# Kernel optimization log

Measured on AMD Instinct MI355X. Metric: run time of the kernel, lower is better.

## Reference

```python
import jax, jax.numpy as jnp
import numpy as np

B, T, H = 4, 8192, 512
LN_EPS = 1e-5


def _ln(x, g, b):
    mu = jnp.mean(x, axis=-1, keepdims=True)
    var = jnp.mean((x - mu) ** 2, axis=-1, keepdims=True)
    return (x - mu) * jax.lax.rsqrt(var + LN_EPS) * g + b


def _log_g(x):
    # log of g(x) = x + 0.5 (x >= 0) else sigmoid(x); both branches NaN-safe.
    return jnp.where(x >= 0, jnp.log(jax.nn.relu(x) + 0.5), -jax.nn.softplus(-x))


def _min_gru(x, Wz, bz, Wh, bh):
    # minGRU parallel log-space scan ("Were RNNs All We Needed?" Alg.), h_0 = 0.
    k = x @ Wz + bz                      # [B,T,H] gate pre-activation
    log_z = -jax.nn.softplus(-k)         # log sigmoid(k)
    log_coeffs = -jax.nn.softplus(k)     # log (1 - sigmoid(k))
    log_tilde_h = _log_g(x @ Wh + bh)
    log_h0 = jnp.full((x.shape[0], 1, x.shape[2]), jnp.log(0.5), x.dtype)  # g(0)=0.5
    log_values = jnp.concatenate([log_h0, log_z + log_tilde_h], axis=1)   # [B,T+1,H]
    a_star = jnp.cumsum(jnp.pad(log_coeffs, ((0, 0), (1, 0), (0, 0))), axis=1)
    log_h = a_star + jax.lax.cumlogsumexp(log_values - a_star, axis=1)
    return jnp.exp(log_h)[:, 1:]         # drop h_0 slot -> [B,T,H]


def setup_inputs() -> dict:
    key = jax.random.key(0)
    ks = jax.random.split(key, 5)
    s = 1.0 / np.sqrt(H)
    return {
        "x": jax.random.normal(ks[0], (B, T, H), jnp.float32),
        "ln1_g": jnp.ones((H,), jnp.float32),
        "ln1_b": jnp.zeros((H,), jnp.float32),
        "Wz": jax.random.normal(ks[1], (H, H), jnp.float32) * s,
        "bz": jnp.zeros((H,), jnp.float32),
        "Wh": jax.random.normal(ks[2], (H, H), jnp.float32) * s,
        "bh": jnp.zeros((H,), jnp.float32),
        "ln2_g": jnp.ones((H,), jnp.float32),
        "ln2_b": jnp.zeros((H,), jnp.float32),
        "W1": jax.random.normal(ks[3], (H, H), jnp.float32) * s,
        "b1": jnp.zeros((H,), jnp.float32),
        "W2": jax.random.normal(ks[4], (H, H), jnp.float32) * s,
        "b2": jnp.zeros((H,), jnp.float32),
    }


def reference(x, ln1_g, ln1_b, Wz, bz, Wh, bh, ln2_g, ln2_b, W1, b1, W2, b2):
    # x = x + minGRU(ln_1(x))   (dropout=0 -> identity)
    x = x + _min_gru(_ln(x, ln1_g, ln1_b), Wz, bz, Wh, bh)
    # x = x + FFN(ln_2(x)) ; FFN = Linear -> ReLU -> Linear (hidden->hidden)
    h = jax.nn.relu(_ln(x, ln2_g, ln2_b) @ W1 + b1)
    x = x + (h @ W2 + b2)
    return x
```

## Files before the change

### kernel.cpp

```cpp
#include <hip/hip_runtime.h>

typedef unsigned short u16;
typedef unsigned int u32;
typedef __bf16 bf16x8 __attribute__((ext_vector_type(8)));
typedef float f32x4 __attribute__((ext_vector_type(4)));
typedef u16 u16x8 __attribute__((ext_vector_type(8)));

__device__ __forceinline__ u16 f2bf(float f) {
    union { float f; u32 i; } v; v.f = f;
    u32 x = v.i;
    u32 r = (x + 0x7fffu + ((x >> 16) & 1u)) >> 16;
    return (u16)r;
}
__device__ __forceinline__ float bf2f(u16 u) {
    union { u32 i; float f; } v; v.i = ((u32)u) << 16; return v.f;
}

__device__ __forceinline__ void gld16(const void* g, void* l) {
    __builtin_amdgcn_global_load_lds(
        (const __attribute__((address_space(1))) void*)g,
        (__attribute__((address_space(3))) void*)l, 16, 0, 0);
}

__global__ __launch_bounds__(256) void transpose4(
    const float* __restrict__ s0, const float* __restrict__ s1,
    const float* __restrict__ s2, const float* __restrict__ s3,
    u16* __restrict__ d0, u16* __restrict__ d1,
    u16* __restrict__ d2, u16* __restrict__ d3)
{
    int bx = blockIdx.x;
    int mat = bx >> 8;
    int tile = bx & 255;
    int tx = (tile & 15) * 32;
    int ty = (tile >> 4) * 32;
    const float* src = (mat == 0) ? s0 : (mat == 1) ? s1 : (mat == 2) ? s2 : s3;
    u16* dst = (mat == 0) ? d0 : (mat == 1) ? d1 : (mat == 2) ? d2 : d3;

    __shared__ u16 tl[32][33];
    int col = threadIdx.x & 31;
    int r8  = threadIdx.x >> 5;
    #pragma unroll
    for (int k = 0; k < 4; ++k) {
        int rr = r8 + k * 8;
        tl[rr][col] = f2bf(src[(ty + rr) * 512 + tx + col]);
    }
    __syncthreads();
    #pragma unroll
    for (int k = 0; k < 4; ++k) {
        int rr = r8 + k * 8;
        dst[(tx + rr) * 512 + ty + col] = tl[col][rr];
    }
}

__global__ __launch_bounds__(256) void ln_k(
    const float* __restrict__ x, const float* __restrict__ g,
    const float* __restrict__ b, u16* __restrict__ y, int rows)
{
    int gid = blockIdx.x * blockDim.x + threadIdx.x;
    int row = gid >> 6;
    int lane = gid & 63;
    if (row >= rows) return;

    const float* xr = x + (size_t)row * 512 + lane * 8;
    float4 a0 = *(const float4*)xr;
    float4 a1 = *(const float4*)(xr + 4);
    float f[8] = {a0.x, a0.y, a0.z, a0.w, a1.x, a1.y, a1.z, a1.w};
    float s = 0.f, s2 = 0.f;
    #pragma unroll
    for (int e = 0; e < 8; ++e) { s += f[e]; s2 += f[e] * f[e]; }
    #pragma unroll
    for (int o = 32; o > 0; o >>= 1) { s += __shfl_xor(s, o); s2 += __shfl_xor(s2, o); }
    const float inv = 1.0f / 512.0f;
    float mean = s * inv;
    float var  = s2 * inv - mean * mean;
    float rstd = rsqrtf(var + 1e-5f);

    float4 g0 = *(const float4*)(g + lane * 8);
    float4 g1 = *(const float4*)(g + lane * 8 + 4);
    float4 b0 = *(const float4*)(b + lane * 8);
    float4 b1 = *(const float4*)(b + lane * 8 + 4);
    float gg[8] = {g0.x, g0.y, g0.z, g0.w, g1.x, g1.y, g1.z, g1.w};
    float bb[8] = {b0.x, b0.y, b0.z, b0.w, b1.x, b1.y, b1.z, b1.w};
    u16x8 ov;
    #pragma unroll
    for (int e = 0; e < 8; ++e)
        ov[e] = f2bf((f[e] - mean) * rstd * gg[e] + bb[e]);
    *(u16x8*)(y + (size_t)row * 512 + lane * 8) = ov;
}

template <int MODE>
__global__ __launch_bounds__(256, 2) void gemm_bt(
    const u16* __restrict__ A, const u16* __restrict__ Bt0,
    const u16* __restrict__ Bt1, const float* __restrict__ bias0,
    const float* __restrict__ bias1, const float* __restrict__ resid,
    void* __restrict__ out0v, u16* __restrict__ out1)
{
    constexpr int Kd = 512, Nd = 512;
    __shared__ __align__(16) u16 As[128 * 32];
    __shared__ __align__(16) u16 Bs0[128 * 32];
    __shared__ __align__(16) u16 Bs1[(MODE == 0) ? 128 * 32 : 8];

    int bx = blockIdx.x;
    bx = (bx & 7) * 128 + (bx >> 3);
    int m0 = (bx >> 2) * 128;
    int n0 = (bx & 3) * 128;
    int tid = threadIdx.x;
    int lane = tid & 63;
    int w = tid >> 6;
    int wm = w & 1, wn = w >> 1;
    int l16 = lane & 15;
    int quad = lane >> 4;

    f32x4 acc0[4][4] = {};
    f32x4 acc1[4][4] = {};

    int ch0 = tid, ch1 = tid + 256;
    int row0 = ch0 >> 2, row1 = ch1 >> 2;
    int g0 = (ch0 & 3) ^ ((ch0 >> 3) & 3);
    int g1 = (ch1 & 3) ^ ((ch1 >> 3) & 3);
    const u16* a0p  = A   + (size_t)(m0 + row0) * Kd + g0 * 8;
    const u16* a1p  = A   + (size_t)(m0 + row1) * Kd + g1 * 8;
    const u16* b00p = Bt0 + (size_t)(n0 + row0) * Kd + g0 * 8;
    const u16* b01p = Bt0 + (size_t)(n0 + row1) * Kd + g1 * 8;
    const u16* b10p = (MODE == 0) ? Bt1 + (size_t)(n0 + row0) * Kd + g0 * 8 : nullptr;
    const u16* b11p = (MODE == 0) ? Bt1 + (size_t)(n0 + row1) * Kd + g1 * 8 : nullptr;

    for (int kt = 0; kt < Kd / 32; ++kt) {
        int k0 = kt * 32;
        gld16(a0p  + k0, &As [ch0 * 8]);
        gld16(a1p  + k0, &As [ch1 * 8]);
        gld16(b00p + k0, &Bs0[ch0 * 8]);
        gld16(b01p + k0, &Bs0[ch1 * 8]);
        if (MODE == 0) {
            gld16(b10p + k0, &Bs1[ch0 * 8]);
            gld16(b11p + k0, &Bs1[ch1 * 8]);
        }
        __syncthreads();

        bf16x8 af[4], bf0[4], bf1[4];
        #pragma unroll
        for (int i = 0; i < 4; ++i) {
            int ra = wm * 64 + i * 16 + l16;
            int rb = wn * 64 + i * 16 + l16;
            int ga = quad ^ ((ra >> 1) & 3);
            int gb = quad ^ ((rb >> 1) & 3);
            af[i]  = *(const bf16x8*)&As [ra * 32 + ga * 8];
            bf0[i] = *(const bf16x8*)&Bs0[rb * 32 + gb * 8];
            if (MODE == 0)
                bf1[i] = *(const bf16x8*)&Bs1[rb * 32 + gb * 8];
        }
        #pragma unroll
        for (int i = 0; i < 4; ++i)
            #pragma unroll
            for (int j = 0; j < 4; ++j) {
                acc0[i][j] = __builtin_amdgcn_mfma_f32_16x16x32_bf16(af[i], bf0[j], acc0[i][j], 0, 0, 0);
                if (MODE == 0)
                    acc1[i][j] = __builtin_amdgcn_mfma_f32_16x16x32_bf16(af[i], bf1[j], acc1[i][j], 0, 0, 0);
            }
        __syncthreads();
    }

    #pragma unroll
    for (int j = 0; j < 4; ++j) {
        int col = n0 + wn * 64 + j * 16 + l16;
        float b0 = bias0[col];
        float b1v = (MODE == 0) ? bias1[col] : 0.f;
        #pragma unroll
        for (int i = 0; i < 4; ++i) {
            #pragma unroll
            for (int r = 0; r < 4; ++r) {
                int row = m0 + wm * 64 + i * 16 + quad * 4 + r;
                size_t off = (size_t)row * Nd + col;
                float v0 = acc0[i][j][r] + b0;
                if (MODE == 0) {
                    ((u16*)out0v)[off] = f2bf(v0);
                    out1[off] = f2bf(acc1[i][j][r] + b1v);
                } else if (MODE == 1) {
                    ((u16*)out0v)[off] = f2bf(fmaxf(v0, 0.f));
                } else {
                    ((float*)out0v)[off] = v0 + resid[off];
                }
            }
        }
    }
}

__device__ __forceinline__ void gate_cv(u16 kraw, u16 hraw, float& c, float& v) {
    float kk = bf2f(kraw);
    float hh = bf2f(hraw);
    float z = 1.f / (1.f + __expf(-kk));
    c = 1.f / (1.f + __expf(kk));
    float gg = (hh >= 0.f) ? (hh + 0.5f) : 1.f / (1.f + __expf(-hh));
    v = z * gg;
}

__global__ __launch_bounds__(256) void scanA(
    const u16* __restrict__ kb, const u16* __restrict__ hp,
    float* __restrict__ chC, float* __restrict__ chV)
{
    int gid = blockIdx.x * 256 + threadIdx.x;
    int h = gid & 511;
    int rest = gid >> 9;
    int b = rest & 3;
    int ch = rest >> 2;
    size_t base = ((size_t)(b * 8192 + ch * 32)) * 512 + h;
    float C = 1.f, V = 0.f;
    #pragma unroll 8
    for (int t = 0; t < 32; ++t) {
        float c, v;
        gate_cv(kb[base + (size_t)t * 512], hp[base + (size_t)t * 512], c, v);
        C *= c;
        V = fmaf(c, V, v);
    }
    int s = b * 512 + h;
    chC[ch * 2048 + s] = C;
    chV[ch * 2048 + s] = V;
}

__global__ __launch_bounds__(256) void scanB1(
    const float* __restrict__ chC, const float* __restrict__ chV,
    float* __restrict__ scC, float* __restrict__ scV)
{
    int gid = blockIdx.x * 256 + threadIdx.x;
    int s = gid & 2047;
    int sc = gid >> 11;
    float C = 1.f, V = 0.f;
    #pragma unroll 4
    for (int i = 0; i < 16; ++i) {
        int ch = sc * 16 + i;
        float c = chC[ch * 2048 + s];
        float v = chV[ch * 2048 + s];
        C *= c;
        V = fmaf(c, V, v);
    }
    scC[sc * 2048 + s] = C;
    scV[sc * 2048 + s] = V;
}

__global__ __launch_bounds__(256) void scanB2(
    const float* __restrict__ scC, const float* __restrict__ scV,
    float* __restrict__ sst)
{
    int s = blockIdx.x * 256 + threadIdx.x;
    float hcur = 0.5f;
    #pragma unroll
    for (int sc = 0; sc < 16; ++sc) {
        sst[sc * 2048 + s] = hcur;
        hcur = fmaf(scC[sc * 2048 + s], hcur, scV[sc * 2048 + s]);
    }
}

__global__ __launch_bounds__(256) void scanB3(
    const float* __restrict__ chC, const float* __restrict__ chV,
    const float* __restrict__ sst, float* __restrict__ hst)
{
    int gid = blockIdx.x * 256 + threadIdx.x;
    int s = gid & 2047;
    int sc = gid >> 11;
    float hcur = sst[sc * 2048 + s];
    #pragma unroll 4
    for (int i = 0; i < 16; ++i) {
        int ch = sc * 16 + i;
        hst[ch * 2048 + s] = hcur;
        hcur = fmaf(chC[ch * 2048 + s], hcur, chV[ch * 2048 + s]);
    }
}

__global__ __launch_bounds__(256) void scanC(
    const u16* __restrict__ kb, const u16* __restrict__ hp,
    const float* __restrict__ hst, const float* __restrict__ x,
    float* __restrict__ x2)
{
    int gid = blockIdx.x * 256 + threadIdx.x;
    int h = gid & 511;
    int rest = gid >> 9;
    int b = rest & 3;
    int ch = rest >> 2;
    size_t base = ((size_t)(b * 8192 + ch * 32)) * 512 + h;
    float hcur = hst[ch * 2048 + b * 512 + h];
    #pragma unroll 8
    for (int t = 0; t < 32; ++t) {
        float c, v;
        size_t off = base + (size_t)t * 512;
        gate_cv(kb[off], hp[off], c, v);
        hcur = fmaf(c, hcur, v);
        x2[off] = x[off] + hcur;
    }
}

extern "C" void kernel_launch(void* const* d_in, const int* in_sizes, int n_in,
                              void* d_out, int out_size, void* d_ws, size_t ws_size,
                              hipStream_t stream)
{
    const float* x    = (const float*)d_in[0];
    const float* ln1g = (const float*)d_in[1];
    const float* ln1b = (const float*)d_in[2];
    const float* Wz   = (const float*)d_in[3];
    const float* bz   = (const float*)d_in[4];
    const float* Wh   = (const float*)d_in[5];
    const float* bh   = (const float*)d_in[6];
    const float* ln2g = (const float*)d_in[7];
    const float* ln2b = (const float*)d_in[8];
    const float* W1   = (const float*)d_in[9];
    const float* b1   = (const float*)d_in[10];
    const float* W2   = (const float*)d_in[11];
    const float* b2   = (const float*)d_in[12];
    float* out = (float*)d_out;

    char* ws = (char*)d_ws;
    constexpr size_t MB = 1024 * 1024;
    u16* Wzt = (u16*)(ws);
    u16* Wht = Wzt + 262144;
    u16* W1t = Wzt + 524288;
    u16* W2t = Wzt + 786432;
    u16* a  = (u16*)(ws + 3 * MB + 512 * 1024);
    u16* kb = (u16*)(ws + 35 * MB + 512 * 1024);
    u16* hp = (u16*)(ws + 67 * MB + 512 * 1024);
    float* chC = (float*)(ws + 3 * MB + 512 * 1024);
    float* chV = chC + 524288;
    float* hst = chV + 524288;
    float* scC = hst + 524288;
    float* scV = scC + 32768;
    float* sst = scV + 32768;

    transpose4<<<1024, 256, 0, stream>>>(Wz, Wh, W1, W2, Wzt, Wht, W1t, W2t);
    ln_k<<<8192, 256, 0, stream>>>(x, ln1g, ln1b, a, 32768);
    gemm_bt<0><<<1024, 256, 0, stream>>>(a, Wzt, Wht, bz, bh, nullptr, kb, hp);
    scanA<<<2048, 256, 0, stream>>>(kb, hp, chC, chV);
    scanB1<<<128, 256, 0, stream>>>(chC, chV, scC, scV);
    scanB2<<<8, 256, 0, stream>>>(scC, scV, sst);
    scanB3<<<128, 256, 0, stream>>>(chC, chV, sst, hst);
    scanC<<<2048, 256, 0, stream>>>(kb, hp, hst, x, out);
    ln_k<<<8192, 256, 0, stream>>>(out, ln2g, ln2b, a, 32768);
    gemm_bt<1><<<1024, 256, 0, stream>>>(a, W1t, nullptr, b1, nullptr, nullptr, kb, nullptr);
    gemm_bt<2><<<1024, 256, 0, stream>>>(kb, W2t, nullptr, b2, nullptr, out, out, nullptr);
}
```

Baseline: 338.5 us.

## Replace GEMM with 256x256-tile double-buffered 8-wave pipelined kernel

```diff
diff --git a/kernel.cpp b/kernel.cpp
--- a/kernel.cpp
+++ b/kernel.cpp
@@ -88,97 +88,109 @@
     *(u16x8*)(y + (size_t)row * 512 + lane * 8) = ov;
 }
 
-template <int MODE>
-__global__ __launch_bounds__(256, 2) void gemm_bt(
-    const u16* __restrict__ A, const u16* __restrict__ Bt0,
-    const u16* __restrict__ Bt1, const float* __restrict__ bias0,
-    const float* __restrict__ bias1, const float* __restrict__ resid,
-    void* __restrict__ out0v, u16* __restrict__ out1)
+template <int EPI>
+__global__ __launch_bounds__(512, 2) void gemm8(
+    const u16* __restrict__ A, const u16* __restrict__ Bt,
+    const float* __restrict__ bias, const float* __restrict__ resid,
+    void* __restrict__ outv)
 {
     constexpr int Kd = 512, Nd = 512;
-    __shared__ __align__(16) u16 As[128 * 32];
-    __shared__ __align__(16) u16 Bs0[128 * 32];
-    __shared__ __align__(16) u16 Bs1[(MODE == 0) ? 128 * 32 : 8];
-
-    int bx = blockIdx.x;
-    bx = (bx & 7) * 128 + (bx >> 3);
-    int m0 = (bx >> 2) * 128;
-    int n0 = (bx & 3) * 128;
+    __shared__ __align__(16) u16 lds[65536];
+
+    int bid = blockIdx.x;
+    int bx = (bid & 7) * 32 + (bid >> 3);
+    int m0 = (bx >> 1) * 256;
+    int n0 = (bx & 1) * 256;
+
     int tid = threadIdx.x;
     int lane = tid & 63;
     int w = tid >> 6;
-    int wm = w & 1, wn = w >> 1;
-    int l16 = lane & 15;
-    int quad = lane >> 4;
-
-    f32x4 acc0[4][4] = {};
-    f32x4 acc1[4][4] = {};
-
-    int ch0 = tid, ch1 = tid + 256;
-    int row0 = ch0 >> 2, row1 = ch1 >> 2;
-    int g0 = (ch0 & 3) ^ ((ch0 >> 3) & 3);
-    int g1 = (ch1 & 3) ^ ((ch1 >> 3) & 3);
-    const u16* a0p  = A   + (size_t)(m0 + row0) * Kd + g0 * 8;
-    const u16* a1p  = A   + (size_t)(m0 + row1) * Kd + g1 * 8;
-    const u16* b00p = Bt0 + (size_t)(n0 + row0) * Kd + g0 * 8;
-    const u16* b01p = Bt0 + (size_t)(n0 + row1) * Kd + g1 * 8;
-    const u16* b10p = (MODE == 0) ? Bt1 + (size_t)(n0 + row0) * Kd + g0 * 8 : nullptr;
-    const u16* b11p = (MODE == 0) ? Bt1 + (size_t)(n0 + row1) * Kd + g1 * 8 : nullptr;
-
-    for (int kt = 0; kt < Kd / 32; ++kt) {
-        int k0 = kt * 32;
-        gld16(a0p  + k0, &As [ch0 * 8]);
-        gld16(a1p  + k0, &As [ch1 * 8]);
-        gld16(b00p + k0, &Bs0[ch0 * 8]);
-        gld16(b01p + k0, &Bs0[ch1 * 8]);
-        if (MODE == 0) {
-            gld16(b10p + k0, &Bs1[ch0 * 8]);
-            gld16(b11p + k0, &Bs1[ch1 * 8]);
-        }
-        __syncthreads();
-
-        bf16x8 af[4], bf0[4], bf1[4];
-        #pragma unroll
-        for (int i = 0; i < 4; ++i) {
-            int ra = wm * 64 + i * 16 + l16;
-            int rb = wn * 64 + i * 16 + l16;
-            int ga = quad ^ ((ra >> 1) & 3);
-            int gb = quad ^ ((rb >> 1) & 3);
-            af[i]  = *(const bf16x8*)&As [ra * 32 + ga * 8];
-            bf0[i] = *(const bf16x8*)&Bs0[rb * 32 + gb * 8];
-            if (MODE == 0)
-                bf1[i] = *(const bf16x8*)&Bs1[rb * 32 + gb * 8];
-        }
-        #pragma unroll
-        for (int i = 0; i < 4; ++i)
-            #pragma unroll
-            for (int j = 0; j < 4; ++j) {
-                acc0[i][j] = __builtin_amdgcn_mfma_f32_16x16x32_bf16(af[i], bf0[j], acc0[i][j], 0, 0, 0);
-                if (MODE == 0)
-                    acc1[i][j] = __builtin_amdgcn_mfma_f32_16x16x32_bf16(af[i], bf1[j], acc1[i][j], 0, 0, 0);
-            }
-        __syncthreads();
-    }
+    int wm = w >> 2, wn = w & 3;
+    int l16 = lane & 15, quad = lane >> 4;
+
+    int sr = tid & 255;
+    int sg = tid >> 8;
+    const u16* aS = A  + (size_t)(m0 + sr) * Kd + sg * 8;
+    const u16* bS = Bt + (size_t)(n0 + sr) * Kd + sg * 8;
+    int dA = sg * 2048 + sr * 8;
+    int dB = 32768 + sg * 2048 + sr * 8;
+
+    int aRd = quad * 2048 + (wm * 128 + l16) * 8;
+    int bRd = 32768 + quad * 2048 + (wn * 64 + l16) * 8;
+
+    f32x4 acc[8][4] = {};
+    bf16x8 bfr[2][4];
+
+#define STAGE_A(tt, h) { int s_ = (tt) & 1; const u16* p_ = aS + (tt) * 64 + (h) * 32; \
+    gld16(p_,      &lds[s_ * 16384 + (h) * 8192 + dA]); \
+    gld16(p_ + 16, &lds[s_ * 16384 + (h) * 8192 + dA + 4096]); }
+#define STAGE_B(tt, h) { int s_ = (tt) & 1; const u16* p_ = bS + (tt) * 64 + (h) * 32; \
+    gld16(p_,      &lds[s_ * 16384 + (h) * 8192 + dB]); \
+    gld16(p_ + 16, &lds[s_ * 16384 + (h) * 8192 + dB + 4096]); }
+
+#define PH(ks, ih, LOADB, ...) { \
+    int fb_ = s * 16384 + (ks) * 8192; \
+    bf16x8 af[4]; \
+    _Pragma("unroll") \
+    for (int ii = 0; ii < 4; ++ii) \
+        af[ii] = *(const bf16x8*)&lds[fb_ + aRd + (ih) * 512 + ii * 128]; \
+    if (LOADB) { \
+        _Pragma("unroll") \
+        for (int j = 0; j < 4; ++j) \
+            bfr[ks][j] = *(const bf16x8*)&lds[fb_ + bRd + j * 128]; \
+    } \
+    __VA_ARGS__; \
+    asm volatile("s_waitcnt vmcnt(6)" ::: "memory"); \
+    __builtin_amdgcn_s_barrier(); \
+    __builtin_amdgcn_s_setprio(1); \
+    _Pragma("unroll") \
+    for (int ii = 0; ii < 4; ++ii) { \
+        _Pragma("unroll") \
+        for (int j = 0; j < 4; ++j) \
+            acc[(ih) * 4 + ii][j] = __builtin_amdgcn_mfma_f32_16x16x32_bf16( \
+                af[ii], bfr[ks][j], acc[(ih) * 4 + ii][j], 0, 0, 0); \
+    } \
+    __builtin_amdgcn_s_setprio(0); \
+    __builtin_amdgcn_sched_barrier(0); \
+    __builtin_amdgcn_s_barrier(); \
+}
+
+    STAGE_B(0, 0); STAGE_A(0, 0); STAGE_B(0, 1); STAGE_A(0, 1);
+    STAGE_B(1, 0); STAGE_A(1, 0); STAGE_B(1, 1);
+    asm volatile("s_waitcnt vmcnt(6)" ::: "memory");
+    __builtin_amdgcn_s_barrier();
+
+    for (int t = 0; t < 8; ++t) {
+        int s = t & 1;
+        PH(0, 0, 1, STAGE_A((t + 1) & 7, 1));
+        PH(0, 1, 0, STAGE_B((t + 2) & 7, 0));
+        PH(1, 0, 1, STAGE_A((t + 2) & 7, 0));
+        PH(1, 1, 0, STAGE_B((t + 2) & 7, 1));
+    }
+#undef PH
+#undef STAGE_A
+#undef STAGE_B
+
+    asm volatile("s_waitcnt vmcnt(0)" ::: "memory");
+    __builtin_amdgcn_s_barrier();
 
     #pragma unroll
     for (int j = 0; j < 4; ++j) {
         int col = n0 + wn * 64 + j * 16 + l16;
-        float b0 = bias0[col];
-        float b1v = (MODE == 0) ? bias1[col] : 0.f;
+        float bv = bias[col];
         #pragma unroll
-        for (int i = 0; i < 4; ++i) {
+        for (int i = 0; i < 8; ++i) {
             #pragma unroll
             for (int r = 0; r < 4; ++r) {
-                int row = m0 + wm * 64 + i * 16 + quad * 4 + r;
+                int row = m0 + wm * 128 + i * 16 + quad * 4 + r;
                 size_t off = (size_t)row * Nd + col;
-                float v0 = acc0[i][j][r] + b0;
-                if (MODE == 0) {
-                    ((u16*)out0v)[off] = f2bf(v0);
-                    out1[off] = f2bf(acc1[i][j][r] + b1v);
-                } else if (MODE == 1) {
-                    ((u16*)out0v)[off] = f2bf(fmaxf(v0, 0.f));
+                float v = acc[i][j][r] + bv;
+                if (EPI == 0) {
+                    ((u16*)outv)[off] = f2bf(v);
+                } else if (EPI == 1) {
+                    ((u16*)outv)[off] = f2bf(fmaxf(v, 0.f));
                 } else {
-                    ((float*)out0v)[off] = v0 + resid[off];
+                    ((float*)outv)[off] = v + resid[off];
                 }
             }
         }
@@ -325,13 +337,14 @@
 
     transpose4<<<1024, 256, 0, stream>>>(Wz, Wh, W1, W2, Wzt, Wht, W1t, W2t);
     ln_k<<<8192, 256, 0, stream>>>(x, ln1g, ln1b, a, 32768);
-    gemm_bt<0><<<1024, 256, 0, stream>>>(a, Wzt, Wht, bz, bh, nullptr, kb, hp);
+    gemm8<0><<<256, 512, 0, stream>>>(a, Wzt, bz, nullptr, kb);
+    gemm8<0><<<256, 512, 0, stream>>>(a, Wht, bh, nullptr, hp);
     scanA<<<2048, 256, 0, stream>>>(kb, hp, chC, chV);
     scanB1<<<128, 256, 0, stream>>>(chC, chV, scC, scV);
     scanB2<<<8, 256, 0, stream>>>(scC, scV, sst);
     scanB3<<<128, 256, 0, stream>>>(chC, chV, sst, hst);
     scanC<<<2048, 256, 0, stream>>>(kb, hp, hst, x, out);
     ln_k<<<8192, 256, 0, stream>>>(out, ln2g, ln2b, a, 32768);
-    gemm_bt<1><<<1024, 256, 0, stream>>>(a, W1t, nullptr, b1, nullptr, nullptr, kb, nullptr);
-    gemm_bt<2><<<1024, 256, 0, stream>>>(kb, W2t, nullptr, b2, nullptr, out, out, nullptr);
-}
+    gemm8<1><<<256, 512, 0, stream>>>(a, W1t, b1, nullptr, kb);
+    gemm8<2><<<256, 512, 0, stream>>>(kb, W2t, b2, out, out);
+}
```

Measured after the change: 396.1 us. 17.0% more time.

## Fuse LN2 into scan output pass and stage GEMM epilogues through LDS

Applied to the files above, without the earlier changes.

```diff
diff --git a/kernel.cpp b/kernel.cpp
--- a/kernel.cpp
+++ b/kernel.cpp
@@ -96,9 +96,11 @@
     void* __restrict__ out0v, u16* __restrict__ out1)
 {
     constexpr int Kd = 512, Nd = 512;
-    __shared__ __align__(16) u16 As[128 * 32];
-    __shared__ __align__(16) u16 Bs0[128 * 32];
-    __shared__ __align__(16) u16 Bs1[(MODE == 0) ? 128 * 32 : 8];
+    constexpr int SMEM_N = (MODE == 2) ? 32768 : 16384;
+    __shared__ __align__(16) u16 smem[SMEM_N];
+    u16* As  = smem;
+    u16* Bs0 = smem + 4096;
+    u16* Bs1 = smem + 8192;
 
     int bx = blockIdx.x;
     bx = (bx & 7) * 128 + (bx >> 3);
@@ -160,27 +162,71 @@
         __syncthreads();
     }
 
-    #pragma unroll
-    for (int j = 0; j < 4; ++j) {
-        int col = n0 + wn * 64 + j * 16 + l16;
-        float b0 = bias0[col];
-        float b1v = (MODE == 0) ? bias1[col] : 0.f;
-        #pragma unroll
-        for (int i = 0; i < 4; ++i) {
+    if (MODE != 2) {
+        u16* Cs = smem;
+        #pragma unroll
+        for (int j = 0; j < 4; ++j) {
+            float bv = bias0[n0 + wn * 64 + j * 16 + l16];
             #pragma unroll
-            for (int r = 0; r < 4; ++r) {
-                int row = m0 + wm * 64 + i * 16 + quad * 4 + r;
-                size_t off = (size_t)row * Nd + col;
-                float v0 = acc0[i][j][r] + b0;
-                if (MODE == 0) {
-                    ((u16*)out0v)[off] = f2bf(v0);
-                    out1[off] = f2bf(acc1[i][j][r] + b1v);
-                } else if (MODE == 1) {
-                    ((u16*)out0v)[off] = f2bf(fmaxf(v0, 0.f));
-                } else {
-                    ((float*)out0v)[off] = v0 + resid[off];
+            for (int i = 0; i < 4; ++i)
+                #pragma unroll
+                for (int r = 0; r < 4; ++r) {
+                    float v = acc0[i][j][r] + bv;
+                    if (MODE == 1) v = fmaxf(v, 0.f);
+                    Cs[(wm * 64 + i * 16 + quad * 4 + r) * 128 + wn * 64 + j * 16 + l16] = f2bf(v);
                 }
+        }
+        __syncthreads();
+        #pragma unroll
+        for (int k = 0; k < 8; ++k) {
+            int c = tid + k * 256;
+            int row = c >> 4, c8 = c & 15;
+            *(u16x8*)((u16*)out0v + (size_t)(m0 + row) * Nd + n0 + c8 * 8) =
+                *(const u16x8*)&Cs[row * 128 + c8 * 8];
+        }
+        if (MODE == 0) {
+            __syncthreads();
+            #pragma unroll
+            for (int j = 0; j < 4; ++j) {
+                float bv = bias1[n0 + wn * 64 + j * 16 + l16];
+                #pragma unroll
+                for (int i = 0; i < 4; ++i)
+                    #pragma unroll
+                    for (int r = 0; r < 4; ++r)
+                        Cs[(wm * 64 + i * 16 + quad * 4 + r) * 128 + wn * 64 + j * 16 + l16] =
+                            f2bf(acc1[i][j][r] + bv);
             }
+            __syncthreads();
+            #pragma unroll
+            for (int k = 0; k < 8; ++k) {
+                int c = tid + k * 256;
+                int row = c >> 4, c8 = c & 15;
+                *(u16x8*)(out1 + (size_t)(m0 + row) * Nd + n0 + c8 * 8) =
+                    *(const u16x8*)&Cs[row * 128 + c8 * 8];
+            }
+        }
+    } else {
+        float* Cf = (float*)smem;
+        #pragma unroll
+        for (int j = 0; j < 4; ++j) {
+            float bv = bias0[n0 + wn * 64 + j * 16 + l16];
+            #pragma unroll
+            for (int i = 0; i < 4; ++i)
+                #pragma unroll
+                for (int r = 0; r < 4; ++r)
+                    Cf[(wm * 64 + i * 16 + quad * 4 + r) * 128 + wn * 64 + j * 16 + l16] =
+                        acc0[i][j][r] + bv;
+        }
+        __syncthreads();
+        #pragma unroll
+        for (int k = 0; k < 16; ++k) {
+            int c = tid + k * 256;
+            int row = c >> 5, c4 = (c & 31) * 4;
+            size_t off = (size_t)(m0 + row) * Nd + n0 + c4;
+            float4 v = *(const float4*)&Cf[row * 128 + c4];
+            const float4 rz = *(const float4*)(resid + off);
+            v.x += rz.x; v.y += rz.y; v.z += rz.z; v.w += rz.w;
+            *(float4*)((float*)out0v + off) = v;
         }
     }
 }
@@ -266,25 +312,53 @@
     }
 }
 
-__global__ __launch_bounds__(256) void scanC(
+__global__ __launch_bounds__(512) void scanC_ln(
     const u16* __restrict__ kb, const u16* __restrict__ hp,
     const float* __restrict__ hst, const float* __restrict__ x,
-    float* __restrict__ x2)
-{
-    int gid = blockIdx.x * 256 + threadIdx.x;
-    int h = gid & 511;
-    int rest = gid >> 9;
-    int b = rest & 3;
-    int ch = rest >> 2;
+    const float* __restrict__ g, const float* __restrict__ bia,
+    float* __restrict__ x2, u16* __restrict__ aout)
+{
+    int h = threadIdx.x;
+    int bx = blockIdx.x;
+    int b = bx >> 8;
+    int ch = bx & 255;
     size_t base = ((size_t)(b * 8192 + ch * 32)) * 512 + h;
     float hcur = hst[ch * 2048 + b * 512 + h];
-    #pragma unroll 8
+
+    float xv[32];
+    #pragma unroll
     for (int t = 0; t < 32; ++t) {
         float c, v;
         size_t off = base + (size_t)t * 512;
         gate_cv(kb[off], hp[off], c, v);
         hcur = fmaf(c, hcur, v);
-        x2[off] = x[off] + hcur;
+        xv[t] = x[off] + hcur;
+    }
+
+    __shared__ float sP[32][8], s2P[32][8];
+    int lane = h & 63, w = h >> 6;
+    #pragma unroll
+    for (int t = 0; t < 32; ++t) {
+        float s = xv[t], s2 = xv[t] * xv[t];
+        #pragma unroll
+        for (int o = 32; o > 0; o >>= 1) { s += __shfl_xor(s, o); s2 += __shfl_xor(s2, o); }
+        if (lane == 0) { sP[t][w] = s; s2P[t][w] = s2; }
+    }
+    __syncthreads();
+
+    float gg = g[h], bb = bia[h];
+    const float inv = 1.0f / 512.0f;
+    #pragma unroll
+    for (int t = 0; t < 32; ++t) {
+        float s = 0.f, s2 = 0.f;
+        #pragma unroll
+        for (int k = 0; k < 8; ++k) { s += sP[t][k]; s2 += s2P[t][k]; }
+        float mean = s * inv;
+        float var  = s2 * inv - mean * mean;
+        float rstd = rsqrtf(var + 1e-5f);
+        size_t off = base + (size_t)t * 512;
+        x2[off] = xv[t];
+        aout[off] = f2bf((xv[t] - mean) * rstd * gg + bb);
     }
 }
 
@@ -330,8 +404,7 @@
     scanB1<<<128, 256, 0, stream>>>(chC, chV, scC, scV);
     scanB2<<<8, 256, 0, stream>>>(scC, scV, sst);
     scanB3<<<128, 256, 0, stream>>>(chC, chV, sst, hst);
-    scanC<<<2048, 256, 0, stream>>>(kb, hp, hst, x, out);
-    ln_k<<<8192, 256, 0, stream>>>(out, ln2g, ln2b, a, 32768);
-    gemm_bt<1><<<1024, 256, 0, stream>>>(a, W1t, nullptr, b1, nullptr, nullptr, kb, nullptr);
-    gemm_bt<2><<<1024, 256, 0, stream>>>(kb, W2t, nullptr, b2, nullptr, out, out, nullptr);
-}
+    scanC_ln<<<1024, 512, 0, stream>>>(kb, hp, hst, x, ln2g, ln2b, out, kb);
+    gemm_bt<1><<<1024, 256, 0, stream>>>(kb, W1t, nullptr, b1, nullptr, nullptr, a, nullptr);
+    gemm_bt<2><<<1024, 256, 0, stream>>>(a, W2t, nullptr, b2, nullptr, out, out, nullptr);
+}
```

After: 397.0 us. 17.3% more time.

## Fuse gate activations and chunk-level scan reduction into the gate GEMM epilogue

Applied to the files above, without the earlier changes.

```diff
diff --git a/kernel.cpp b/kernel.cpp
--- a/kernel.cpp
+++ b/kernel.cpp
@@ -14,6 +14,12 @@
 }
 __device__ __forceinline__ float bf2f(u16 u) {
     union { u32 i; float f; } v; v.i = ((u32)u) << 16; return v.f;
+}
+__device__ __forceinline__ u16 f2h(float f) {
+    union { _Float16 h; u16 u; } v; v.h = (_Float16)f; return v.u;
+}
+__device__ __forceinline__ float h2f(u16 u) {
+    union { _Float16 h; u16 u; } v; v.u = u; return (float)v.h;
 }
 
 __device__ __forceinline__ void gld16(const void* g, void* l) {
@@ -93,12 +99,15 @@
     const u16* __restrict__ A, const u16* __restrict__ Bt0,
     const u16* __restrict__ Bt1, const float* __restrict__ bias0,
     const float* __restrict__ bias1, const float* __restrict__ resid,
-    void* __restrict__ out0v, u16* __restrict__ out1)
+    void* __restrict__ out0v, u16* __restrict__ out1,
+    float* __restrict__ chCp, float* __restrict__ chVp)
 {
     constexpr int Kd = 512, Nd = 512;
-    __shared__ __align__(16) u16 As[128 * 32];
-    __shared__ __align__(16) u16 Bs0[128 * 32];
-    __shared__ __align__(16) u16 Bs1[(MODE == 0) ? 128 * 32 : 8];
+    constexpr int SMEM_N = (MODE == 0) ? 34816 : 8192;
+    __shared__ __align__(16) u16 smem[SMEM_N];
+    u16* As  = smem;
+    u16* Bs0 = smem + 4096;
+    u16* Bs1 = smem + 8192;
 
     int bx = blockIdx.x;
     bx = (bx & 7) * 128 + (bx >> 3);
@@ -160,62 +169,82 @@
         __syncthreads();
     }
 
-    #pragma unroll
-    for (int j = 0; j < 4; ++j) {
-        int col = n0 + wn * 64 + j * 16 + l16;
-        float b0 = bias0[col];
-        float b1v = (MODE == 0) ? bias1[col] : 0.f;
-        #pragma unroll
-        for (int i = 0; i < 4; ++i) {
+    if (MODE == 0) {
+        u16* Cc = smem;
+        u16* Cv = smem + 17408;
+        #pragma unroll
+        for (int j = 0; j < 4; ++j) {
+            int col = n0 + wn * 64 + j * 16 + l16;
+            float bk = bias0[col];
+            float bhv = bias1[col];
             #pragma unroll
-            for (int r = 0; r < 4; ++r) {
-                int row = m0 + wm * 64 + i * 16 + quad * 4 + r;
-                size_t off = (size_t)row * Nd + col;
-                float v0 = acc0[i][j][r] + b0;
-                if (MODE == 0) {
-                    ((u16*)out0v)[off] = f2bf(v0);
-                    out1[off] = f2bf(acc1[i][j][r] + b1v);
-                } else if (MODE == 1) {
-                    ((u16*)out0v)[off] = f2bf(fmaxf(v0, 0.f));
-                } else {
-                    ((float*)out0v)[off] = v0 + resid[off];
+            for (int i = 0; i < 4; ++i)
+                #pragma unroll
+                for (int r = 0; r < 4; ++r) {
+                    int lr = wm * 64 + i * 16 + quad * 4 + r;
+                    int lc = wn * 64 + j * 16 + l16;
+                    float kk = acc0[i][j][r] + bk;
+                    float hh = acc1[i][j][r] + bhv;
+                    float z = 1.f / (1.f + __expf(-kk));
+                    float c = 1.f / (1.f + __expf(kk));
+                    float gg = (hh >= 0.f) ? (hh + 0.5f) : 1.f / (1.f + __expf(-hh));
+                    Cc[lr * 136 + lc] = f2h(c);
+                    Cv[lr * 136 + lc] = f2h(z * gg);
+                }
+        }
+        __syncthreads();
+        u16* cb = (u16*)out0v;
+        #pragma unroll
+        for (int k = 0; k < 8; ++k) {
+            int c = tid + k * 256;
+            int row = c >> 4, c8 = c & 15;
+            size_t off = (size_t)(m0 + row) * Nd + n0 + c8 * 8;
+            *(u16x8*)(cb   + off) = *(const u16x8*)&Cc[row * 136 + c8 * 8];
+            *(u16x8*)(out1 + off) = *(const u16x8*)&Cv[row * 136 + c8 * 8];
+        }
+        int h2 = tid & 127;
+        #pragma unroll
+        for (int u = 0; u < 2; ++u) {
+            int cc = (tid >> 7) + u * 2;
+            float C = 1.f, V = 0.f;
+            #pragma unroll 8
+            for (int t = 0; t < 32; ++t) {
+                int lr = cc * 32 + t;
+                float c = h2f(Cc[lr * 136 + h2]);
+                float v = h2f(Cv[lr * 136 + h2]);
+                C *= c;
+                V = fmaf(c, V, v);
+            }
+            int g_row = m0 + cc * 32;
+            int b = g_row >> 13;
+            int chgl = (g_row & 8191) >> 5;
+            int idx = chgl * 2048 + b * 512 + n0 + h2;
+            chCp[idx] = C;
+            chVp[idx] = V;
+        }
+    } else {
+        #pragma unroll
+        for (int j = 0; j < 4; ++j) {
+            int col = n0 + wn * 64 + j * 16 + l16;
+            float b0 = bias0[col];
+            #pragma unroll
+            for (int i = 0; i < 4; ++i) {
+                #pragma unroll
+                for (int r = 0; r < 4; ++r) {
+                    int row = m0 + wm * 64 + i * 16 + quad * 4 + r;
+                    size_t off = (size_t)row * Nd + col;
+                    float v0 = acc0[i][j][r] + b0;
+                    if (MODE == 1) {
+                        ((u16*)out0v)[off] = f2bf(fmaxf(v0, 0.f));
+                    } else {
+                        ((float*)out0v)[off] = v0 + resid[off];
+                    }
                 }
             }
         }
     }
 }
 
-__device__ __forceinline__ void gate_cv(u16 kraw, u16 hraw, float& c, float& v) {
-    float kk = bf2f(kraw);
-    float hh = bf2f(hraw);
-    float z = 1.f / (1.f + __expf(-kk));
-    c = 1.f / (1.f + __expf(kk));
-    float gg = (hh >= 0.f) ? (hh + 0.5f) : 1.f / (1.f + __expf(-hh));
-    v = z * gg;
-}
-
-__global__ __launch_bounds__(256) void scanA(
-    const u16* __restrict__ kb, const u16* __restrict__ hp,
-    float* __restrict__ chC, float* __restrict__ chV)
-{
-    int gid = blockIdx.x * 256 + threadIdx.x;
-    int h = gid & 511;
-    int rest = gid >> 9;
-    int b = rest & 3;
-    int ch = rest >> 2;
-    size_t base = ((size_t)(b * 8192 + ch * 32)) * 512 + h;
-    float C = 1.f, V = 0.f;
-    #pragma unroll 8
-    for (int t = 0; t < 32; ++t) {
-        float c, v;
-        gate_cv(kb[base + (size_t)t * 512], hp[base + (size_t)t * 512], c, v);
-        C *= c;
-        V = fmaf(c, V, v);
-    }
-    int s = b * 512 + h;
-    chC[ch * 2048 + s] = C;
-    chV[ch * 2048 + s] = V;
-}
 
 __global__ __launch_bounds__(256) void scanB1(
     const float* __restrict__ chC, const float* __restrict__ chV,
@@ -267,7 +296,7 @@
 }
 
 __global__ __launch_bounds__(256) void scanC(
-    const u16* __restrict__ kb, const u16* __restrict__ hp,
+    const u16* __restrict__ cb, const u16* __restrict__ vb,
     const float* __restrict__ hst, const float* __restrict__ x,
     float* __restrict__ x2)
 {
@@ -280,9 +309,9 @@
     float hcur = hst[ch * 2048 + b * 512 + h];
     #pragma unroll 8
     for (int t = 0; t < 32; ++t) {
-        float c, v;
         size_t off = base + (size_t)t * 512;
-        gate_cv(kb[off], hp[off], c, v);
+        float c = h2f(cb[off]);
+        float v = h2f(vb[off]);
         hcur = fmaf(c, hcur, v);
         x2[off] = x[off] + hcur;
     }
@@ -314,24 +343,23 @@
     u16* W1t = Wzt + 524288;
     u16* W2t = Wzt + 786432;
     u16* a  = (u16*)(ws + 3 * MB + 512 * 1024);
-    u16* kb = (u16*)(ws + 35 * MB + 512 * 1024);
-    u16* hp = (u16*)(ws + 67 * MB + 512 * 1024);
-    float* chC = (float*)(ws + 3 * MB + 512 * 1024);
-    float* chV = chC + 524288;
-    float* hst = chV + 524288;
+    u16* cb = (u16*)(ws + 35 * MB + 512 * 1024);
+    u16* vb = (u16*)(ws + 67 * MB + 512 * 1024);
+    float* hst = (float*)(ws + 3 * MB + 512 * 1024);
     float* scC = hst + 524288;
     float* scV = scC + 32768;
     float* sst = scV + 32768;
+    float* chC = (float*)d_out;
+    float* chV = chC + 524288;
 
     transpose4<<<1024, 256, 0, stream>>>(Wz, Wh, W1, W2, Wzt, Wht, W1t, W2t);
     ln_k<<<8192, 256, 0, stream>>>(x, ln1g, ln1b, a, 32768);
-    gemm_bt<0><<<1024, 256, 0, stream>>>(a, Wzt, Wht, bz, bh, nullptr, kb, hp);
-    scanA<<<2048, 256, 0, stream>>>(kb, hp, chC, chV);
+    gemm_bt<0><<<1024, 256, 0, stream>>>(a, Wzt, Wht, bz, bh, nullptr, cb, vb, chC, chV);
     scanB1<<<128, 256, 0, stream>>>(chC, chV, scC, scV);
     scanB2<<<8, 256, 0, stream>>>(scC, scV, sst);
     scanB3<<<128, 256, 0, stream>>>(chC, chV, sst, hst);
-    scanC<<<2048, 256, 0, stream>>>(kb, hp, hst, x, out);
+    scanC<<<2048, 256, 0, stream>>>(cb, vb, hst, x, out);
     ln_k<<<8192, 256, 0, stream>>>(out, ln2g, ln2b, a, 32768);
-    gemm_bt<1><<<1024, 256, 0, stream>>>(a, W1t, nullptr, b1, nullptr, nullptr, kb, nullptr);
-    gemm_bt<2><<<1024, 256, 0, stream>>>(kb, W2t, nullptr, b2, nullptr, out, out, nullptr);
-}
+    gemm_bt<1><<<1024, 256, 0, stream>>>(a, W1t, nullptr, b1, nullptr, nullptr, cb, nullptr, nullptr, nullptr);
+    gemm_bt<2><<<1024, 256, 0, stream>>>(cb, W2t, nullptr, b2, nullptr, out, out, nullptr, nullptr, nullptr);
+}
```

Result: faster. 314.0 us (-7.2%).
